# Kernel optimization log

Measured on AMD Instinct MI355X. Metric: run time of the kernel, lower is better.

## Reference

```python
import jax, jax.numpy as jnp
import numpy as np

LAMBDA = 0.5
ALPHA_PRE = 1.0
ALPHA_DA = 1.0

B, N, C, T, O = 8, 1024, 64, 12, 64


def setup_inputs() -> dict:
    key = jax.random.key(0)
    ks = jax.random.split(key, 10)
    s = 0.1  # keep tanh out of deep saturation, like xavier-init scales
    return {
        "x": jax.random.normal(ks[0], (B, N, C, T), dtype=jnp.float32),
        "static_adj": jax.random.uniform(ks[1], (N, N), dtype=jnp.float32) / N,
        "W0": jax.random.normal(ks[2], (C, O), dtype=jnp.float32) * s,
        "b0": jax.random.normal(ks[3], (O,), dtype=jnp.float32) * s,
        "Ws": jax.random.normal(ks[4], (T, C, O), dtype=jnp.float32) * s,
        "bs": jax.random.normal(ks[5], (T, O), dtype=jnp.float32) * s,
        "Wd": jax.random.normal(ks[6], (T, C, O), dtype=jnp.float32) * s,
        "bd": jax.random.normal(ks[7], (T, O), dtype=jnp.float32) * s,
        "E1": jax.random.normal(ks[8], (T, N, O), dtype=jnp.float32) * s,
        "E2": jax.random.normal(ks[9], (T, N, O), dtype=jnp.float32) * s,
    }


def reference(x, static_adj, W0, b0, Ws, bs, Wd, bd, E1, E2):
    # x: [B,N,C,T] -> [T,B,N,C] so the per-timestep layers vectorize over leading T.
    xt = jnp.transpose(x, (3, 0, 1, 2))  # [T,B,N,C]
    n = xt.shape[2]

    # shared top-level linear
    x0 = jnp.einsum('tbnc,co->tbno', xt, W0) + b0  # [T,B,N,O]

    # static GCN per timestep: linear(static_adj @ x_t)
    sagg = jnp.einsum('nm,tbmc->tbnc', static_adj, xt)
    static_out = jnp.einsum('tbnc,tco->tbno', sagg, Ws) + bs[:, None, None, :]

    # dynamic GCN: base = linear_t(x_t)
    base = jnp.einsum('tbnc,tco->tbno', xt, Wd) + bd[:, None, None, :]
    DE1 = jnp.tanh(ALPHA_PRE * (base * E1[:, None]))  # [T,B,N,O]
    DE2 = jnp.tanh(ALPHA_PRE * (base * E2[:, None]))
    # cross = DE1@DE2^T - DE2@DE1^T = M - M^T
    M = jnp.einsum('tbno,tbmo->tbnm', DE1, DE2)  # [T,B,N,N]
    DA = jax.nn.relu(jnp.tanh(ALPHA_DA * (M - jnp.swapaxes(M, -1, -2))))

    # symmetric degree normalization of (DA + I)
    DA = DA + jnp.eye(n, dtype=DA.dtype)
    rowsum = jnp.clip(DA.sum(axis=-1), 1e-12, None)
    d_inv_sqrt = rowsum ** -0.5
    DA = DA * d_inv_sqrt[..., :, None] * d_inv_sqrt[..., None, :]

    dagg = jnp.einsum('tbnm,tbmc->tbnc', DA, xt)
    dyn_out = jnp.einsum('tbnc,tco->tbno', dagg, Wd) + bd[:, None, None, :]

    fused = (LAMBDA - 0.025) * static_out + (1.0 - LAMBDA - 0.025) * dyn_out + 0.05 * x0
    return jnp.transpose(fused, (1, 2, 3, 0))  # [B,N,O,T]
```

## Files before the change

kernel.cpp:

```cpp
#include <hip/hip_runtime.h>

#define BB 8
#define NN 1024
#define CC 64
#define TT 12
#define OO 64

typedef unsigned short u16;
typedef __attribute__((ext_vector_type(8))) short s16x8;
typedef __attribute__((ext_vector_type(4))) float f32x4;
typedef __attribute__((ext_vector_type(4))) unsigned int u32x4;
typedef __attribute__((ext_vector_type(2))) unsigned int u32x2;

__device__ __forceinline__ u16 f2bu(float f){
  union { float f; unsigned u; } v; v.f = f;
  unsigned r = v.u + 0x7FFFu + ((v.u >> 16) & 1u);
  return (u16)(r >> 16);
}
__device__ __forceinline__ float b2f(u16 h){
  union { unsigned u; float f; } v; v.u = ((unsigned)h) << 16; return v.f;
}
__device__ __forceinline__ float relu_tanh(float d){
  float e = __expf(2.0f * d);
  return fmaxf(1.0f - 2.0f * __builtin_amdgcn_rcpf(e + 1.0f), 0.0f);
}
__device__ __forceinline__ float tanh_fast(float d){
  float e = __expf(2.0f * d);
  return 1.0f - 2.0f * __builtin_amdgcn_rcpf(e + 1.0f);
}
__device__ __forceinline__ float tanh_sgn(float x){
  float ax = fabsf(x);
  float e = __expf(2.0f * ax);
  float t = 1.0f - 2.0f * __builtin_amdgcn_rcpf(e + 1.0f);
  return x < 0.0f ? -t : t;
}

#define MFMA16(a,b,c) __builtin_amdgcn_mfma_f32_16x16x32_bf16((a),(b),(c),0,0,0)

__device__ __forceinline__ s16x8 ld72(const u16* s, int row0, int ko, int lane){
  return *(const s16x8*)(s + (row0 + (lane & 15)) * 72 + ko + ((lane >> 4) << 3));
}

__global__ __launch_bounds__(256) void k0_transpose(const float* __restrict__ x,
                                                    u16* __restrict__ xt){
  const int n = blockIdx.x, b = blockIdx.y;
  __shared__ float s[CC*TT];
  const float* src = x + (size_t)(b*NN + n)*CC*TT;
  for (int k = threadIdx.x; k < CC*TT; k += 256) s[k] = src[k];
  __syncthreads();
  for (int k = threadIdx.x; k < CC*TT; k += 256){
    const int t = k >> 6, c = k & 63;
    xt[(((size_t)t*BB + b)*NN + n)*CC + c] = f2bu(s[c*TT + t]);
  }
}

__global__ __launch_bounds__(256) void kadj(const float* __restrict__ adj,
                                            u16* __restrict__ adjb){
  const size_t i = ((size_t)blockIdx.x*256 + threadIdx.x)*4;
  const float4 v = *(const float4*)(adj + i);
  u16 o0=f2bu(v.x), o1=f2bu(v.y), o2=f2bu(v.z), o3=f2bu(v.w);
  adjb[i]=o0; adjb[i+1]=o1; adjb[i+2]=o2; adjb[i+3]=o3;
}

__global__ __launch_bounds__(256) void kinit(float* __restrict__ rs){
  const size_t i = (size_t)blockIdx.x*256 + threadIdx.x;
  if (i < (size_t)TT*BB*NN) rs[i] = 1.0f;
}

__global__ __launch_bounds__(256) void k1_de(const u16* __restrict__ xt,
    const float* __restrict__ Wd, const float* __restrict__ bd,
    const float* __restrict__ E1, const float* __restrict__ E2,
    u16* __restrict__ DE1g, u16* __restrict__ DE2g){
  __shared__ __align__(16) u16 sWd[64*72];
  const int tid = threadIdx.x, lane = tid & 63, wid = tid >> 6;
  const int l15 = lane & 15, lr4 = lane >> 4;
  const int it = blockIdx.x, b = blockIdx.y, t = blockIdx.z;
  const int n0 = it * 64;
  for (int k = tid; k < 4096; k += 256){
    const int o = k & 63, c = k >> 6;
    sWd[o*72 + c] = f2bu(Wd[(size_t)t*4096 + c*64 + o]);
  }
  __syncthreads();
  const size_t tb = (size_t)t*BB + b;
  const u16* gx = xt + (tb*NN + n0)*CC;
  const int wrow = wid * 16;
  const f32x4 fz = {0.f,0.f,0.f,0.f};
  f32x4 acc[4] = {fz, fz, fz, fz};
  #pragma unroll
  for (int ks = 0; ks < 2; ++ks){
    const int ko = ks*32;
    const s16x8 a = *(const s16x8*)(gx + (wrow + l15)*CC + ko + (lr4 << 3));
    #pragma unroll
    for (int v = 0; v < 4; ++v)
      acc[v] = MFMA16(a, ld72(sWd, v*16, ko, lane), acc[v]);
  }
  #pragma unroll
  for (int v = 0; v < 4; ++v){
    const int o = v*16 + l15;
    const float bdv = bd[t*OO + o];
    #pragma unroll
    for (int e = 0; e < 4; ++e){
      const int n = n0 + wrow + (lr4 << 2) + e;
      const float base = acc[v][e] + bdv;
      const size_t eo = ((size_t)t*NN + n)*OO + o;
      const size_t so = (tb*NN + n)*OO + o;
      DE1g[so] = f2bu(tanh_sgn(base * E1[eo]));
      DE2g[so] = f2bu(tanh_sgn(base * E2[eo]));
    }
  }
}

__global__ __launch_bounds__(256) void k2a(const u16* __restrict__ DE1g,
    const u16* __restrict__ DE2g, float* __restrict__ rowsum){
  __shared__ __align__(16) u16 s1A[64*72], s2nA[64*72];
  __shared__ __align__(16) u16 s1B[64*72], s2nB[64*72];
  const int tid = threadIdx.x, lane = tid & 63, wid = tid >> 6;
  const int l15 = lane & 15, lr4 = lane >> 4;
  const int nwg = 8*BB*TT;
  const int logical = ((int)blockIdx.x & 7)*(nwg >> 3) + ((int)blockIdx.x >> 3);
  const int p = logical & 7;
  const size_t tb = (size_t)(logical >> 3);
  const int tiA = p, tiB = 15 - p;
  const u16* g1 = DE1g + tb*NN*OO;
  const u16* g2 = DE2g + tb*NN*OO;
  for (int k = tid; k < 512; k += 256){
    const int r = k >> 3, c = (k & 7) << 3;
    *(s16x8*)(s1A + r*72 + c) = *(const s16x8*)(g1 + (size_t)(tiA*64 + r)*OO + c);
    s16x8 vA = *(const s16x8*)(g2 + (size_t)(tiA*64 + r)*OO + c);
    u32x4 wA = *(u32x4*)&vA; wA ^= 0x80008000u;
    *(u32x4*)(s2nA + r*72 + c) = wA;
    *(s16x8*)(s1B + r*72 + c) = *(const s16x8*)(g1 + (size_t)(tiB*64 + r)*OO + c);
    s16x8 vB = *(const s16x8*)(g2 + (size_t)(tiB*64 + r)*OO + c);
    u32x4 wB = *(u32x4*)&vB; wB ^= 0x80008000u;
    *(u32x4*)(s2nB + r*72 + c) = wB;
  }
  __syncthreads();
  const int wrow = wid * 16;
  s16x8 a1A[2], na2A[2], a1B[2], na2B[2];
  #pragma unroll
  for (int ks = 0; ks < 2; ++ks){
    a1A[ks]  = ld72(s1A,  wrow, ks*32, lane);
    na2A[ks] = ld72(s2nA, wrow, ks*32, lane);
    a1B[ks]  = ld72(s1B,  wrow, ks*32, lane);
    na2B[ks] = ld72(s2nB, wrow, ks*32, lane);
  }
  u16* sJ1 = s1A;
  u16* sJ2 = s2nA;
  const int srow = tid >> 2, sc0 = (tid & 3) << 4;
  s16x8 pB1a,pB1b, pB2a,pB2b;
#define LOADT(TJ) do { \
    pB1a = *(const s16x8*)(g2 + (size_t)((TJ)*64 + srow)*OO + sc0); \
    pB1b = *(const s16x8*)(g2 + (size_t)((TJ)*64 + srow)*OO + sc0 + 8); \
    pB2a = *(const s16x8*)(g1 + (size_t)((TJ)*64 + srow)*OO + sc0); \
    pB2b = *(const s16x8*)(g1 + (size_t)((TJ)*64 + srow)*OO + sc0 + 8); \
  } while (0)
  LOADT(p);
  float rpA[4] = {0.f,0.f,0.f,0.f}, rpB[4] = {0.f,0.f,0.f,0.f};
  const f32x4 fz = {0.f,0.f,0.f,0.f};
  float* rsg = rowsum + tb*NN;
  __syncthreads();
  for (int tj = p; tj < 16; ++tj){
    *(s16x8*)(sJ1 + srow*72 + sc0)     = pB1a;
    *(s16x8*)(sJ1 + srow*72 + sc0 + 8) = pB1b;
    *(s16x8*)(sJ2 + srow*72 + sc0)     = pB2a;
    *(s16x8*)(sJ2 + srow*72 + sc0 + 8) = pB2b;
    __syncthreads();
    if (tj < 15) LOADT(tj + 1);
    s16x8 b1[4], b2[4], b1h[4], b2h[4];
    #pragma unroll
    for (int v = 0; v < 4; ++v){
      b1[v]  = ld72(sJ1, v*16, 0,  lane);
      b2[v]  = ld72(sJ2, v*16, 0,  lane);
      b1h[v] = ld72(sJ1, v*16, 32, lane);
      b2h[v] = ld72(sJ2, v*16, 32, lane);
    }
    {
      f32x4 z[4];
      #pragma unroll
      for (int v = 0; v < 4; ++v){
        z[v] = MFMA16(a1A[0],  b1[v],  fz);
        z[v] = MFMA16(na2A[0], b2[v],  z[v]);
        z[v] = MFMA16(a1A[1],  b1h[v], z[v]);
        z[v] = MFMA16(na2A[1], b2h[v], z[v]);
      }
      float colp[4] = {0.f,0.f,0.f,0.f};
      #pragma unroll
      for (int v = 0; v < 4; ++v)
        #pragma unroll
        for (int e = 0; e < 4; ++e){
          const float th = tanh_fast(z[v][e]);
          rpA[e]  += fmaxf(th, 0.f);
          colp[v] += fmaxf(-th, 0.f);
        }
      if (tj > tiA){
        #pragma unroll
        for (int v = 0; v < 4; ++v){
          float c = colp[v];
          c += __shfl_xor(c, 16); c += __shfl_xor(c, 32);
          if (lane < 16) atomicAdd(&rsg[tj*64 + v*16 + lane], c);
        }
      }
    }
    if (tj >= tiB){
      f32x4 z[4];
      #pragma unroll
      for (int v = 0; v < 4; ++v){
        z[v] = MFMA16(a1B[0],  b1[v],  fz);
        z[v] = MFMA16(na2B[0], b2[v],  z[v]);
        z[v] = MFMA16(a1B[1],  b1h[v], z[v]);
        z[v] = MFMA16(na2B[1], b2h[v], z[v]);
      }
      float colp[4] = {0.f,0.f,0.f,0.f};
      #pragma unroll
      for (int v = 0; v < 4; ++v)
        #pragma unroll
        for (int e = 0; e < 4; ++e){
          const float th = tanh_fast(z[v][e]);
          rpB[e]  += fmaxf(th, 0.f);
          colp[v] += fmaxf(-th, 0.f);
        }
      if (tj > tiB){
        #pragma unroll
        for (int v = 0; v < 4; ++v){
          float c = colp[v];
          c += __shfl_xor(c, 16); c += __shfl_xor(c, 32);
          if (lane < 16) atomicAdd(&rsg[tj*64 + v*16 + lane], c);
        }
      }
    }
    __syncthreads();
  }
#undef LOADT
  #pragma unroll
  for (int e = 0; e < 4; ++e){
    float r = rpA[e];
    r += __shfl_xor(r, 1); r += __shfl_xor(r, 2);
    r += __shfl_xor(r, 4); r += __shfl_xor(r, 8);
    if (l15 == 0) atomicAdd(&rsg[tiA*64 + wrow + (lr4 << 2) + e], r);
  }
  #pragma unroll
  for (int e = 0; e < 4; ++e){
    float r = rpB[e];
    r += __shfl_xor(r, 1); r += __shfl_xor(r, 2);
    r += __shfl_xor(r, 4); r += __shfl_xor(r, 8);
    if (l15 == 0) atomicAdd(&rsg[tiB*64 + wrow + (lr4 << 2) + e], r);
  }
}

__global__ __launch_bounds__(256) void k3b(const u16* __restrict__ xt,
    const float* __restrict__ Wd, const float* __restrict__ Ws,
    const float* __restrict__ W0, const float* __restrict__ bd,
    const float* __restrict__ bs, const float* __restrict__ b0,
    const float* __restrict__ rowsum, u16* __restrict__ xdvT,
    u16* __restrict__ xswT, u16* __restrict__ x0w){
  __shared__ __align__(16) u16 sW[64*72];
  const int tid = threadIdx.x, lane = tid & 63, wid = tid >> 6;
  const int l15 = lane & 15, lr4 = lane >> 4;
  const int it = blockIdx.x, b = blockIdx.y, t = blockIdx.z;
  const size_t tb = (size_t)t*BB + b;
  const int n0 = it * 128, wrow = wid * 32;
  const float* dvb = rowsum + tb*NN + n0;
  float dis[2][4];
  #pragma unroll
  for (int u = 0; u < 2; ++u)
    #pragma unroll
    for (int e = 0; e < 4; ++e)
      dis[u][e] = rsqrtf(dvb[wrow + u*16 + (lr4 << 2) + e]);
  float badd[4];
  #pragma unroll
  for (int v = 0; v < 4; ++v){
    const int o = v*16 + l15;
    badd[v] = 0.475f*(bd[t*OO + o] + bs[t*OO + o]) + 0.05f*b0[o];
  }
  const u16* gx = xt + (tb*NN + n0)*CC;
  const f32x4 fz = {0.f,0.f,0.f,0.f};
  for (int pass = 0; pass < 3; ++pass){
    __syncthreads();
    {
      const float* Wsrc = (pass == 0) ? (Wd + (size_t)t*4096)
                        : (pass == 1) ? (Ws + (size_t)t*4096) : W0;
      const float scale = (pass == 2) ? 0.05f : 0.475f;
      for (int k = tid; k < 4096; k += 256){
        const int o = k & 63, c = k >> 6;
        sW[o*72 + c] = f2bu(scale * Wsrc[c*64 + o]);
      }
    }
    __syncthreads();
    f32x4 acc[2][4];
    #pragma unroll
    for (int u = 0; u < 2; ++u)
      #pragma unroll
      for (int v = 0; v < 4; ++v) acc[u][v] = fz;
    #pragma unroll
    for (int ks = 0; ks < 2; ++ks){
      const int ko = ks*32;
      s16x8 bw[4];
      #pragma unroll
      for (int v = 0; v < 4; ++v) bw[v] = ld72(sW, v*16, ko, lane);
      #pragma unroll
      for (int u = 0; u < 2; ++u){
        const s16x8 a = *(const s16x8*)(gx + (wrow + u*16 + l15)*CC + ko + (lr4 << 3));
        #pragma unroll
        for (int v = 0; v < 4; ++v) acc[u][v] = MFMA16(a, bw[v], acc[u][v]);
      }
    }
    #pragma unroll
    for (int u = 0; u < 2; ++u)
      #pragma unroll
      for (int v = 0; v < 4; ++v){
        const int o = v*16 + l15;
        #pragma unroll
        for (int e = 0; e < 4; ++e){
          const int nl = wrow + u*16 + (lr4 << 2) + e;
          float val = acc[u][v][e];
          if (pass == 0)      xdvT[(tb*OO + o)*NN + n0 + nl] = f2bu(val * dis[u][e]);
          else if (pass == 1) xswT[(tb*OO + o)*NN + n0 + nl] = f2bu(val);
          else                x0w[(tb*NN + n0 + nl)*OO + o]  = f2bu(val + badd[v]);
        }
      }
  }
}

__global__ __launch_bounds__(256) void k4s(const u16* __restrict__ adjb,
    const u16* __restrict__ xswT, u16* __restrict__ outSta){
  __shared__ __align__(16) u16 sJ[64*72], sS[64*72];
  const int tid = threadIdx.x, lane = tid & 63, wid = tid >> 6;
  const int l15 = lane & 15, lr4 = lane >> 4;
  const int nwg = 16*BB*TT;
  const int logical = ((int)blockIdx.x & 7)*(nwg >> 3) + ((int)blockIdx.x >> 3);
  const int ti = logical / (BB*TT);
  const size_t tb = (size_t)(logical % (BB*TT));
  const u16* xs = xswT + tb*OO*NN;
  const int i0 = ti * 64, wrow = wid * 16;
  const int srow = tid >> 2, sc0 = (tid & 3) << 4;
  s16x8 pJa, pJb, pSa, pSb;
#define LOADS(TJ) do { \
    pJa = *(const s16x8*)(adjb + (size_t)(i0 + srow)*NN + (TJ)*64 + sc0); \
    pJb = *(const s16x8*)(adjb + (size_t)(i0 + srow)*NN + (TJ)*64 + sc0 + 8); \
    pSa = *(const s16x8*)(xs   + (size_t)srow*NN + (TJ)*64 + sc0); \
    pSb = *(const s16x8*)(xs   + (size_t)srow*NN + (TJ)*64 + sc0 + 8); \
  } while (0)
  LOADS(0);
  const f32x4 fz = {0.f,0.f,0.f,0.f};
  f32x4 as_[4] = {fz,fz,fz,fz};
  for (int tj = 0; tj < 16; ++tj){
    *(s16x8*)(sJ + srow*72 + sc0)     = pJa;
    *(s16x8*)(sJ + srow*72 + sc0 + 8) = pJb;
    *(s16x8*)(sS + srow*72 + sc0)     = pSa;
    *(s16x8*)(sS + srow*72 + sc0 + 8) = pSb;
    __syncthreads();
    if (tj < 15) LOADS(tj + 1);
    const s16x8 aJ0 = ld72(sJ, wrow, 0,  lane);
    const s16x8 aJ1 = ld72(sJ, wrow, 32, lane);
    #pragma unroll
    for (int v = 0; v < 4; ++v){
      as_[v] = MFMA16(aJ0, ld72(sS, v*16, 0,  lane), as_[v]);
      as_[v] = MFMA16(aJ1, ld72(sS, v*16, 32, lane), as_[v]);
    }
    __syncthreads();
  }
#undef LOADS
  #pragma unroll
  for (int v = 0; v < 4; ++v){
    const int o = v*16 + l15;
    #pragma unroll
    for (int e = 0; e < 4; ++e){
      const int n = i0 + wrow + (lr4 << 2) + e;
      outSta[(tb*NN + n)*OO + o] = f2bu(as_[v][e]);
    }
  }
}

__global__ __launch_bounds__(256) void k2bf(const u16* __restrict__ DE1g,
    const u16* __restrict__ DE2g, const u16* __restrict__ xdvT,
    const float* __restrict__ rowsum, float* __restrict__ outT){
  __shared__ __align__(16) u16 sB1[64*72], sB2[64*72], sXD[64*72];
  const int tid = threadIdx.x, lane = tid & 63, wid = tid >> 6;
  const int l15 = lane & 15, lr4 = lane >> 4;
  const int nwg = 16*BB*TT;
  const int logical = ((int)blockIdx.x & 7)*(nwg >> 3) + ((int)blockIdx.x >> 3);
  const int ti = logical & 15;
  const size_t tb = (size_t)(logical >> 4);
  const u16* g1 = DE1g + tb*NN*OO;
  const u16* g2 = DE2g + tb*NN*OO;
  const u16* xd = xdvT + tb*OO*NN;
  const float* dv = rowsum + tb*NN;
  const int i0 = ti * 64;
  for (int k = tid; k < 512; k += 256){
    const int r = k >> 3, c = (k & 7) << 3;
    *(s16x8*)(sB1 + r*72 + c) = *(const s16x8*)(g1 + (size_t)(i0 + r)*OO + c);
    s16x8 v = *(const s16x8*)(g2 + (size_t)(i0 + r)*OO + c);
    u32x4 w = *(u32x4*)&v; w ^= 0x80008000u;
    *(u32x4*)(sB2 + r*72 + c) = w;
  }
  __syncthreads();
  const int wrow = wid * 16;
  s16x8 a1[2], na2[2];
  #pragma unroll
  for (int ks = 0; ks < 2; ++ks){
    a1[ks]  = ld72(sB1, wrow, ks*32, lane);
    na2[ks] = ld72(sB2, wrow, ks*32, lane);
  }
  const int srow = tid >> 2, sc0 = (tid & 3) << 4;
  const int g0 = sc0 >> 2;
  int kap[4];
  #pragma unroll
  for (int q = 0; q < 4; ++q){
    const int g = g0 + q;
    kap[q] = ((g & 3) << 3) + (((g >> 2) & 1) << 2) + ((g >> 3) << 5);
  }
  s16x8 pB1a,pB1b, pB2a,pB2b, pXDa,pXDb;
#define LOADT(TJ) do { \
    pB1a = *(const s16x8*)(g2 + (size_t)((TJ)*64 + srow)*OO + sc0); \
    pB1b = *(const s16x8*)(g2 + (size_t)((TJ)*64 + srow)*OO + sc0 + 8); \
    pB2a = *(const s16x8*)(g1 + (size_t)((TJ)*64 + srow)*OO + sc0); \
    pB2b = *(const s16x8*)(g1 + (size_t)((TJ)*64 + srow)*OO + sc0 + 8); \
    pXDa = *(const s16x8*)(xd + (size_t)srow*NN + (TJ)*64 + sc0); \
    pXDb = *(const s16x8*)(xd + (size_t)srow*NN + (TJ)*64 + sc0 + 8); \
  } while (0)
  LOADT(0);
  const f32x4 fz = {0.f,0.f,0.f,0.f};
  f32x4 ad[4] = {fz,fz,fz,fz};
  __syncthreads();
  for (int tj = 0; tj < 16; ++tj){
    *(s16x8*)(sB1 + srow*72 + sc0)     = pB1a;
    *(s16x8*)(sB1 + srow*72 + sc0 + 8) = pB1b;
    *(s16x8*)(sB2 + srow*72 + sc0)     = pB2a;
    *(s16x8*)(sB2 + srow*72 + sc0 + 8) = pB2b;
    {
      const u32x4 xa = *(const u32x4*)&pXDa;
      const u32x4 xb = *(const u32x4*)&pXDb;
      u32x2 h;
      h[0] = xa[0]; h[1] = xa[1];
      *(u32x2*)(sXD + srow*72 + kap[0]) = h;
      h[0] = xa[2]; h[1] = xa[3];
      *(u32x2*)(sXD + srow*72 + kap[1]) = h;
      h[0] = xb[0]; h[1] = xb[1];
      *(u32x2*)(sXD + srow*72 + kap[2]) = h;
      h[0] = xb[2]; h[1] = xb[3];
      *(u32x2*)(sXD + srow*72 + kap[3]) = h;
    }
    __syncthreads();
    if (tj < 15) LOADT(tj + 1);
    f32x4 y[4];
    #pragma unroll
    for (int v = 0; v < 4; ++v){
      y[v] = MFMA16(ld72(sB1, v*16, 0,  lane), a1[0],  fz);
      y[v] = MFMA16(ld72(sB2, v*16, 0,  lane), na2[0], y[v]);
      y[v] = MFMA16(ld72(sB1, v*16, 32, lane), a1[1],  y[v]);
      y[v] = MFMA16(ld72(sB2, v*16, 32, lane), na2[1], y[v]);
    }
    float q[4][4];
    #pragma unroll
    for (int v = 0; v < 4; ++v)
      #pragma unroll
      for (int e = 0; e < 4; ++e)
        q[v][e] = relu_tanh(y[v][e]);
    u32x4 w0, w1;
    asm("v_cvt_pk_bf16_f32 %0, %1, %2" : "=v"(w0[0]) : "v"(q[0][0]), "v"(q[0][1]));
    asm("v_cvt_pk_bf16_f32 %0, %1, %2" : "=v"(w0[1]) : "v"(q[0][2]), "v"(q[0][3]));
    asm("v_cvt_pk_bf16_f32 %0, %1, %2" : "=v"(w0[2]) : "v"(q[1][0]), "v"(q[1][1]));
    asm("v_cvt_pk_bf16_f32 %0, %1, %2" : "=v"(w0[3]) : "v"(q[1][2]), "v"(q[1][3]));
    asm("v_cvt_pk_bf16_f32 %0, %1, %2" : "=v"(w1[0]) : "v"(q[2][0]), "v"(q[2][1]));
    asm("v_cvt_pk_bf16_f32 %0, %1, %2" : "=v"(w1[1]) : "v"(q[2][2]), "v"(q[2][3]));
    asm("v_cvt_pk_bf16_f32 %0, %1, %2" : "=v"(w1[2]) : "v"(q[3][0]), "v"(q[3][1]));
    asm("v_cvt_pk_bf16_f32 %0, %1, %2" : "=v"(w1[3]) : "v"(q[3][2]), "v"(q[3][3]));
    const s16x8 pa0 = *(const s16x8*)&w0;
    const s16x8 pa1 = *(const s16x8*)&w1;
    #pragma unroll
    for (int v = 0; v < 4; ++v){
      ad[v] = MFMA16(pa0, ld72(sXD, v*16, 0,  lane), ad[v]);
      ad[v] = MFMA16(pa1, ld72(sXD, v*16, 32, lane), ad[v]);
    }
    __syncthreads();
  }
#undef LOADT
  const int grow0 = i0 + wrow + (lr4 << 2);
  float disv[4];
  #pragma unroll
  for (int e = 0; e < 4; ++e) disv[e] = rsqrtf(dv[grow0 + e]);
  #pragma unroll
  for (int v = 0; v < 4; ++v){
    const int o = v*16 + l15;
    #pragma unroll
    for (int e = 0; e < 4; ++e){
      const float xw = b2f(xd[(size_t)o*NN + grow0 + e]);
      outT[(tb*NN + grow0 + e)*OO + o] = disv[e]*(ad[v][e] + xw);
    }
  }
}

__global__ __launch_bounds__(256) void k5(const float* __restrict__ outT,
                                          const u16* __restrict__ x0w,
                                          const u16* __restrict__ outSta,
                                          float* __restrict__ out){
  __shared__ float s[16*64*12];
  const int tid = threadIdx.x;
  const int nb = blockIdx.x, b = blockIdx.y;
  const int n0 = nb * 16;
  for (int t = 0; t < TT; ++t){
    for (int k = tid; k < 1024; k += 256){
      const int r = k >> 6, o = k & 63;
      const size_t idx = (((size_t)t*BB + b)*NN + n0 + r)*OO + o;
      s[(r*64 + o)*12 + t] = outT[idx] + b2f(x0w[idx]) + b2f(outSta[idx]);
    }
  }
  __syncthreads();
  float* dst = out + (size_t)(b*NN + n0)*OO*TT;
  for (int k = tid; k < 16*64*12; k += 256) dst[k] = s[k];
}

extern "C" void kernel_launch(void* const* d_in, const int* in_sizes, int n_in,
                              void* d_out, int out_size, void* d_ws, size_t ws_size,
                              hipStream_t stream) {
  const float* x   = (const float*)d_in[0];
  const float* adj = (const float*)d_in[1];
  const float* W0  = (const float*)d_in[2];
  const float* b0  = (const float*)d_in[3];
  const float* Ws  = (const float*)d_in[4];
  const float* bs  = (const float*)d_in[5];
  const float* Wd  = (const float*)d_in[6];
  const float* bd  = (const float*)d_in[7];
  const float* E1  = (const float*)d_in[8];
  const float* E2  = (const float*)d_in[9];
  float* out = (float*)d_out;

  char* w = (char*)d_ws;
  size_t off = 0;
  auto take = [&](size_t bytes) -> char* {
    char* p = w + off;
    off += bytes; off = (off + 255) & ~(size_t)255;
    return p;
  };
  const size_t NE = (size_t)TT*BB*NN*OO;
  u16*   xt    = (u16*)  take(NE*2);
  u16*   adjb  = (u16*)  take((size_t)NN*NN*2);
  u16*   DE1   = (u16*)  take(NE*2);
  u16*   DE2   = (u16*)  take(NE*2);
  float* rowsum= (float*)take((size_t)TT*BB*NN*4);
  u16*   xdvT  = (u16*)  take(NE*2);
  u16*   xswT  = (u16*)  take(NE*2);
  u16*   x0w   = (u16*)  take(NE*2);
  u16*   outSta= (u16*)  take(NE*2);
  float* outT  = (float*)take(NE*4);

  k0_transpose<<<dim3(NN, BB), 256, 0, stream>>>(x, xt);
  kadj<<<dim3((NN*NN)/1024), 256, 0, stream>>>(adj, adjb);
  kinit<<<dim3((TT*BB*NN + 255)/256), 256, 0, stream>>>(rowsum);
  k1_de<<<dim3(16, BB, TT), 256, 0, stream>>>(xt, Wd, bd, E1, E2, DE1, DE2);
  k2a<<<dim3(8*BB*TT), 256, 0, stream>>>(DE1, DE2, rowsum);
  k3b<<<dim3(8, BB, TT), 256, 0, stream>>>(xt, Wd, Ws, W0, bd, bs, b0,
                                           rowsum, xdvT, xswT, x0w);
  k4s<<<dim3(16*BB*TT), 256, 0, stream>>>(adjb, xswT, outSta);
  k2bf<<<dim3(16*BB*TT), 256, 0, stream>>>(DE1, DE2, xdvT, rowsum, outT);
  k5<<<dim3(NN/16, BB), 256, 0, stream>>>(outT, x0w, outSta, out);
}
```

Baseline: 219.7 us.

## Process two row strips per workgroup in k2bf to reuse streamed tiles

```diff
diff --git a/kernel.cpp b/kernel.cpp
--- a/kernel.cpp
+++ b/kernel.cpp
@@ -377,29 +377,43 @@
   __shared__ __align__(16) u16 sB1[64*72], sB2[64*72], sXD[64*72];
   const int tid = threadIdx.x, lane = tid & 63, wid = tid >> 6;
   const int l15 = lane & 15, lr4 = lane >> 4;
-  const int nwg = 16*BB*TT;
+  const int nwg = 8*BB*TT;
   const int logical = ((int)blockIdx.x & 7)*(nwg >> 3) + ((int)blockIdx.x >> 3);
-  const int ti = logical & 15;
-  const size_t tb = (size_t)(logical >> 4);
+  const int p = logical & 7;
+  const size_t tb = (size_t)(logical >> 3);
+  const int i0A = p * 64, i0B = (p + 8) * 64;
   const u16* g1 = DE1g + tb*NN*OO;
   const u16* g2 = DE2g + tb*NN*OO;
   const u16* xd = xdvT + tb*OO*NN;
   const float* dv = rowsum + tb*NN;
-  const int i0 = ti * 64;
+  const int wrow = wid * 16;
+  s16x8 a1A[2], na2A[2], a1B[2], na2B[2];
   for (int k = tid; k < 512; k += 256){
     const int r = k >> 3, c = (k & 7) << 3;
-    *(s16x8*)(sB1 + r*72 + c) = *(const s16x8*)(g1 + (size_t)(i0 + r)*OO + c);
-    s16x8 v = *(const s16x8*)(g2 + (size_t)(i0 + r)*OO + c);
+    *(s16x8*)(sB1 + r*72 + c) = *(const s16x8*)(g1 + (size_t)(i0A + r)*OO + c);
+    s16x8 v = *(const s16x8*)(g2 + (size_t)(i0A + r)*OO + c);
     u32x4 w = *(u32x4*)&v; w ^= 0x80008000u;
     *(u32x4*)(sB2 + r*72 + c) = w;
   }
   __syncthreads();
-  const int wrow = wid * 16;
-  s16x8 a1[2], na2[2];
   #pragma unroll
   for (int ks = 0; ks < 2; ++ks){
-    a1[ks]  = ld72(sB1, wrow, ks*32, lane);
-    na2[ks] = ld72(sB2, wrow, ks*32, lane);
+    a1A[ks]  = ld72(sB1, wrow, ks*32, lane);
+    na2A[ks] = ld72(sB2, wrow, ks*32, lane);
+  }
+  __syncthreads();
+  for (int k = tid; k < 512; k += 256){
+    const int r = k >> 3, c = (k & 7) << 3;
+    *(s16x8*)(sB1 + r*72 + c) = *(const s16x8*)(g1 + (size_t)(i0B + r)*OO + c);
+    s16x8 v = *(const s16x8*)(g2 + (size_t)(i0B + r)*OO + c);
+    u32x4 w = *(u32x4*)&v; w ^= 0x80008000u;
+    *(u32x4*)(sB2 + r*72 + c) = w;
+  }
+  __syncthreads();
+  #pragma unroll
+  for (int ks = 0; ks < 2; ++ks){
+    a1B[ks]  = ld72(sB1, wrow, ks*32, lane);
+    na2B[ks] = ld72(sB2, wrow, ks*32, lane);
   }
   const int srow = tid >> 2, sc0 = (tid & 3) << 4;
   const int g0 = sc0 >> 2;
@@ -420,7 +434,7 @@
   } while (0)
   LOADT(0);
   const f32x4 fz = {0.f,0.f,0.f,0.f};
-  f32x4 ad[4] = {fz,fz,fz,fz};
+  f32x4 adA[4] = {fz,fz,fz,fz}, adB[4] = {fz,fz,fz,fz};
   __syncthreads();
   for (int tj = 0; tj < 16; ++tj){
     *(s16x8*)(sB1 + srow*72 + sc0)     = pB1a;
@@ -442,50 +456,67 @@
     }
     __syncthreads();
     if (tj < 15) LOADT(tj + 1);
-    f32x4 y[4];
+    s16x8 jb1[4], jb2[4], jb1h[4], jb2h[4];
     #pragma unroll
     for (int v = 0; v < 4; ++v){
-      y[v] = MFMA16(ld72(sB1, v*16, 0,  lane), a1[0],  fz);
-      y[v] = MFMA16(ld72(sB2, v*16, 0,  lane), na2[0], y[v]);
-      y[v] = MFMA16(ld72(sB1, v*16, 32, lane), a1[1],  y[v]);
-      y[v] = MFMA16(ld72(sB2, v*16, 32, lane), na2[1], y[v]);
-    }
-    float q[4][4];
-    #pragma unroll
-    for (int v = 0; v < 4; ++v)
-      #pragma unroll
-      for (int e = 0; e < 4; ++e)
-        q[v][e] = relu_tanh(y[v][e]);
-    u32x4 w0, w1;
-    asm("v_cvt_pk_bf16_f32 %0, %1, %2" : "=v"(w0[0]) : "v"(q[0][0]), "v"(q[0][1]));
-    asm("v_cvt_pk_bf16_f32 %0, %1, %2" : "=v"(w0[1]) : "v"(q[0][2]), "v"(q[0][3]));
-    asm("v_cvt_pk_bf16_f32 %0, %1, %2" : "=v"(w0[2]) : "v"(q[1][0]), "v"(q[1][1]));
-    asm("v_cvt_pk_bf16_f32 %0, %1, %2" : "=v"(w0[3]) : "v"(q[1][2]), "v"(q[1][3]));
-    asm("v_cvt_pk_bf16_f32 %0, %1, %2" : "=v"(w1[0]) : "v"(q[2][0]), "v"(q[2][1]));
-    asm("v_cvt_pk_bf16_f32 %0, %1, %2" : "=v"(w1[1]) : "v"(q[2][2]), "v"(q[2][3]));
-    asm("v_cvt_pk_bf16_f32 %0, %1, %2" : "=v"(w1[2]) : "v"(q[3][0]), "v"(q[3][1]));
-    asm("v_cvt_pk_bf16_f32 %0, %1, %2" : "=v"(w1[3]) : "v"(q[3][2]), "v"(q[3][3]));
-    const s16x8 pa0 = *(const s16x8*)&w0;
-    const s16x8 pa1 = *(const s16x8*)&w1;
+      jb1[v]  = ld72(sB1, v*16, 0,  lane);
+      jb2[v]  = ld72(sB2, v*16, 0,  lane);
+      jb1h[v] = ld72(sB1, v*16, 32, lane);
+      jb2h[v] = ld72(sB2, v*16, 32, lane);
+    }
+#define STRIP_PV(A1, NA2, AD) do { \
+    f32x4 y[4]; \
+    _Pragma("unroll") \
+    for (int v = 0; v < 4; ++v){ \
+      y[v] = MFMA16(jb1[v],  A1[0],  fz); \
+      y[v] = MFMA16(jb2[v],  NA2[0], y[v]); \
+      y[v] = MFMA16(jb1h[v], A1[1],  y[v]); \
+      y[v] = MFMA16(jb2h[v], NA2[1], y[v]); \
+    } \
+    float q[4][4]; \
+    _Pragma("unroll") \
+    for (int v = 0; v < 4; ++v) \
+      _Pragma("unroll") \
+      for (int e = 0; e < 4; ++e) \
+        q[v][e] = relu_tanh(y[v][e]); \
+    u32x4 w0, w1; \
+    asm("v_cvt_pk_bf16_f32 %0, %1, %2" : "=v"(w0[0]) : "v"(q[0][0]), "v"(q[0][1])); \
+    asm("v_cvt_pk_bf16_f32 %0, %1, %2" : "=v"(w0[1]) : "v"(q[0][2]), "v"(q[0][3])); \
+    asm("v_cvt_pk_bf16_f32 %0, %1, %2" : "=v"(w0[2]) : "v"(q[1][0]), "v"(q[1][1])); \
+    asm("v_cvt_pk_bf16_f32 %0, %1, %2" : "=v"(w0[3]) : "v"(q[1][2]), "v"(q[1][3])); \
+    asm("v_cvt_pk_bf16_f32 %0, %1, %2" : "=v"(w1[0]) : "v"(q[2][0]), "v"(q[2][1])); \
+    asm("v_cvt_pk_bf16_f32 %0, %1, %2" : "=v"(w1[1]) : "v"(q[2][2]), "v"(q[2][3])); \
+    asm("v_cvt_pk_bf16_f32 %0, %1, %2" : "=v"(w1[2]) : "v"(q[3][0]), "v"(q[3][1])); \
+    asm("v_cvt_pk_bf16_f32 %0, %1, %2" : "=v"(w1[3]) : "v"(q[3][2]), "v"(q[3][3])); \
+    const s16x8 pa0 = *(const s16x8*)&w0; \
+    const s16x8 pa1 = *(const s16x8*)&w1; \
+    _Pragma("unroll") \
+    for (int v = 0; v < 4; ++v){ \
+      AD[v] = MFMA16(pa0, ld72(sXD, v*16, 0,  lane), AD[v]); \
+      AD[v] = MFMA16(pa1, ld72(sXD, v*16, 32, lane), AD[v]); \
+    } } while (0)
+    STRIP_PV(a1A, na2A, adA);
+    STRIP_PV(a1B, na2B, adB);
+#undef STRIP_PV
+    __syncthreads();
+  }
+#undef LOADT
+  #pragma unroll
+  for (int s = 0; s < 2; ++s){
+    const int i0 = s ? i0B : i0A;
+    const f32x4* ad = s ? adB : adA;
+    const int grow0 = i0 + wrow + (lr4 << 2);
+    float disv[4];
+    #pragma unroll
+    for (int e = 0; e < 4; ++e) disv[e] = rsqrtf(dv[grow0 + e]);
     #pragma unroll
     for (int v = 0; v < 4; ++v){
-      ad[v] = MFMA16(pa0, ld72(sXD, v*16, 0,  lane), ad[v]);
-      ad[v] = MFMA16(pa1, ld72(sXD, v*16, 32, lane), ad[v]);
-    }
-    __syncthreads();
-  }
-#undef LOADT
-  const int grow0 = i0 + wrow + (lr4 << 2);
-  float disv[4];
-  #pragma unroll
-  for (int e = 0; e < 4; ++e) disv[e] = rsqrtf(dv[grow0 + e]);
-  #pragma unroll
-  for (int v = 0; v < 4; ++v){
-    const int o = v*16 + l15;
-    #pragma unroll
-    for (int e = 0; e < 4; ++e){
-      const float xw = b2f(xd[(size_t)o*NN + grow0 + e]);
-      outT[(tb*NN + grow0 + e)*OO + o] = disv[e]*(ad[v][e] + xw);
+      const int o = v*16 + l15;
+      #pragma unroll
+      for (int e = 0; e < 4; ++e){
+        const float xw = b2f(xd[(size_t)o*NN + grow0 + e]);
+        outT[(tb*NN + grow0 + e)*OO + o] = disv[e]*(ad[v][e] + xw);
+      }
     }
   }
 }
@@ -552,6 +583,6 @@
   k3b<<<dim3(8, BB, TT), 256, 0, stream>>>(xt, Wd, Ws, W0, bd, bs, b0,
                                            rowsum, xdvT, xswT, x0w);
   k4s<<<dim3(16*BB*TT), 256, 0, stream>>>(adjb, xswT, outSta);
-  k2bf<<<dim3(16*BB*TT), 256, 0, stream>>>(DE1, DE2, xdvT, rowsum, outT);
+  k2bf<<<dim3(8*BB*TT), 256, 0, stream>>>(DE1, DE2, xdvT, rowsum, outT);
   k5<<<dim3(NN/16, BB), 256, 0, stream>>>(outT, x0w, outSta, out);
 }
```

Result: no change. 220.7 us (+0.4%).
